# Kernel optimization log

Measured on AMD Instinct MI355X. Metric: run time of the kernel, lower is better.

The kernel has to match this reference:

```python
import jax, jax.numpy as jnp
import numpy as np

IN, H, FC1, FC2, OUT = 3, 30, 64, 32, 1
B, T = 8192, 256


def _lstm_layer(xT, W_ih, W_hh, b_ih, b_hh):
    """xT: (T, B, Din). Returns (hidden sequence (T,B,H), final h (B,H)).
    PyTorch gate order: i, f, g, o."""
    # Precompute input contribution for all timesteps (one big GEMM).
    gx = jnp.einsum('tbd,gd->tbg', xT, W_ih) + b_ih + b_hh  # (T,B,4H)
    b = xT.shape[1]
    h0 = jnp.zeros((b, W_hh.shape[1]), xT.dtype)
    c0 = h0

    def step(carry, g):
        h, c = carry
        gates = g + h @ W_hh.T
        i, f, gg, o = jnp.split(gates, 4, axis=-1)
        i = jax.nn.sigmoid(i)
        f = jax.nn.sigmoid(f)
        gg = jnp.tanh(gg)
        o = jax.nn.sigmoid(o)
        c = f * c + i * gg
        h = o * jnp.tanh(c)
        return (h, c), h

    (h_n, _), ys = jax.lax.scan(step, (h0, c0), gx)
    return ys, h_n


def setup_inputs() -> dict:
    key = jax.random.key(0)
    ks = jax.random.split(key, 16)
    s = 0.18  # ~1/sqrt(hidden_size), matches PyTorch uniform init scale
    inp = {
        'x': jax.random.normal(ks[0], (B, T, IN), jnp.float32),
        'W_ih0': jax.random.normal(ks[1], (4 * H, IN), jnp.float32) * s,
        'W_hh0': jax.random.normal(ks[2], (4 * H, H), jnp.float32) * s,
        'b_ih0': jax.random.normal(ks[3], (4 * H,), jnp.float32) * s,
        'b_hh0': jax.random.normal(ks[4], (4 * H,), jnp.float32) * s,
        'W_ih1': jax.random.normal(ks[5], (4 * H, H), jnp.float32) * s,
        'W_hh1': jax.random.normal(ks[6], (4 * H, H), jnp.float32) * s,
        'b_ih1': jax.random.normal(ks[7], (4 * H,), jnp.float32) * s,
        'b_hh1': jax.random.normal(ks[8], (4 * H,), jnp.float32) * s,
        'W_fc1': jax.random.normal(ks[9], (FC1, H), jnp.float32) * s,
        'b_fc1': jax.random.normal(ks[10], (FC1,), jnp.float32) * s,
        'W_fc2': jax.random.normal(ks[11], (FC2, FC1), jnp.float32) * 0.125,
        'b_fc2': jax.random.normal(ks[12], (FC2,), jnp.float32) * 0.125,
        'W_fc3': jax.random.normal(ks[13], (OUT, FC2), jnp.float32) * 0.17,
        'b_fc3': jax.random.normal(ks[14], (OUT,), jnp.float32) * 0.17,
    }
    return inp


def reference(x, W_ih0, W_hh0, b_ih0, b_hh0, W_ih1, W_hh1, b_ih1, b_hh1,
              W_fc1, b_fc1, W_fc2, b_fc2, W_fc3, b_fc3):
    xT = jnp.swapaxes(x, 0, 1)  # (T,B,IN)
    ys, _ = _lstm_layer(xT, W_ih0, W_hh0, b_ih0, b_hh0)   # layer 0 sequence
    _, h_n = _lstm_layer(ys, W_ih1, W_hh1, b_ih1, b_hh1)  # layer 1 final h
    # FC head (dropout = identity in eval mode)
    z = jax.nn.relu(h_n @ W_fc1.T + b_fc1)
    z = jax.nn.relu(z @ W_fc2.T + b_fc2)
    z = jax.nn.sigmoid(z @ W_fc3.T + b_fc3)
    return z.squeeze(-1)  # (B,)
```

## Files before the change

### kernel.cpp

```cpp
#include <hip/hip_runtime.h>

#define TT   256
#define HID  30
#define LOG2E 1.4426950408889634f
#define HS   40

typedef __bf16 bf16x8_t __attribute__((ext_vector_type(8)));
typedef float  f32x4_t  __attribute__((ext_vector_type(4)));

__device__ __forceinline__ float fexp2(float x){
#if __has_builtin(__builtin_amdgcn_exp2f)
    return __builtin_amdgcn_exp2f(x);
#else
    return exp2f(x);
#endif
}
__device__ __forceinline__ float frcp(float x){
#if __has_builtin(__builtin_amdgcn_rcpf)
    return __builtin_amdgcn_rcpf(x);
#else
    return 1.f/x;
#endif
}
__device__ __forceinline__ float fsigmoid(float x){ return frcp(1.f + fexp2(-LOG2E*x)); }
__device__ __forceinline__ f32x4_t exp4(f32x4_t v){
    f32x4_t e; e[0]=fexp2(v[0]); e[1]=fexp2(v[1]); e[2]=fexp2(v[2]); e[3]=fexp2(v[3]); return e;
}
__device__ __forceinline__ f32x4_t rcp4(f32x4_t v){
    f32x4_t r; r[0]=frcp(v[0]); r[1]=frcp(v[1]); r[2]=frcp(v[2]); r[3]=frcp(v[3]); return r;
}
__device__ __forceinline__ f32x4_t splat4(float v){ f32x4_t r = {v,v,v,v}; return r; }

__device__ __forceinline__ f32x4_t lstm_act(f32x4_t aI, f32x4_t aF, f32x4_t aG,
                                            f32x4_t aO, f32x4_t& cst){
    f32x4_t eI = exp4(aI);
    f32x4_t eF = exp4(aF);
    f32x4_t eG = exp4(aG);
    f32x4_t eO = exp4(aO);
    f32x4_t f  = rcp4(eF + 1.f);
    f32x4_t tG = eG + 1.f;
    f32x4_t p  = (eG - 1.f) * rcp4(eI*tG + tG);
    cst = f*cst + p;
    f32x4_t cc;
    cc[0]=fminf(fmaxf(cst[0],-30.f),30.f);
    cc[1]=fminf(fmaxf(cst[1],-30.f),30.f);
    cc[2]=fminf(fmaxf(cst[2],-30.f),30.f);
    cc[3]=fminf(fmaxf(cst[3],-30.f),30.f);
    f32x4_t eC = exp4(cc * (2.f*LOG2E));
    f32x4_t tC = eC + 1.f;
    return (eC - 1.f) * rcp4(eO*tC + tC);
}

__global__ __launch_bounds__(256, 2)
void lstm_fused(const float* __restrict__ x,
    const float* __restrict__ Wih0, const float* __restrict__ Whh0,
    const float* __restrict__ bih0, const float* __restrict__ bhh0,
    const float* __restrict__ Wih1, const float* __restrict__ Whh1,
    const float* __restrict__ bih1, const float* __restrict__ bhh1,
    const float* __restrict__ Wfc1, const float* __restrict__ bfc1,
    const float* __restrict__ Wfc2, const float* __restrict__ bfc2,
    const float* __restrict__ Wfc3, const float* __restrict__ bfc3,
    float* __restrict__ out)
{
    __shared__ __align__(16) __bf16 h0f[2][16][HS];
    __shared__ __align__(16) __bf16 h1f[2][16][HS];
    __shared__ float h1_last[16*32];
    __shared__ float zbuf[16*64];
    __shared__ float z2buf[16*32];

    const int tid  = threadIdx.x;
    const int lane = tid & 63;
    const int wv   = tid >> 6;
    const int lay  = wv >> 1;
    const int uh   = wv & 1;
    const int n    = lane & 15;
    const int q    = lane >> 4;
    const int q4   = q*4;
    const int u    = uh*16 + n;
    const bool colok = (u < HID);
    const int uq   = colok ? u : 0;
    const int bbase = blockIdx.x * 16;

    bf16x8_t fA[4], fB[4];
    float bv[4], wx[4];
    {
        const float scl[4] = {-LOG2E, -LOG2E, 2.f*LOG2E, -LOG2E};
        #pragma unroll
        for (int g = 0; g < 4; ++g) {
            const int row = g*HID + uq;
            const float sg = scl[g];
            bf16x8_t va{}, vb{};
            #pragma unroll
            for (int j = 0; j < 8; ++j) {
                int k = q*8 + j;
                float wa = 0.f, wb = 0.f;
                if (colok) {
                    if (lay == 0) {
                        if (k < HID)      wa = Whh0[row*HID + k];
                        else if (k < 32)  wa = Wih0[row*3 + (k - HID)];
                    } else {
                        if (k < HID) { wa = Wih1[row*HID + k];  wb = Whh1[row*HID + k]; }
                    }
                }
                va[j] = (__bf16)(sg*wa);
                vb[j] = (__bf16)(sg*wb);
            }
            fA[g] = va;  fB[g] = vb;
            float bb = 0.f, ww = 0.f;
            if (colok) {
                bb = lay ? (bih1[row] + bhh1[row]) : (bih0[row] + bhh0[row]);
                if (lay == 0) ww = Wih0[row*3 + 2];
            }
            bv[g] = sg*bb;  wx[g] = sg*ww;
        }
    }

    f32x4_t cst = {0.f,0.f,0.f,0.f};

    for (int i = tid; i < 2*16*HS; i += 256) {
        (&h0f[0][0][0])[i] = (__bf16)0.f;
        (&h1f[0][0][0])[i] = (__bf16)0.f;
    }
    __syncthreads();
    if (tid < 32) {
        int m = tid >> 1, cc = tid & 1;
        h0f[1][m][30+cc] = (__bf16)x[(size_t)(bbase+m)*(TT*3) + cc];
    }
    __syncthreads();

    const float* xB = x + (size_t)bbase*(TT*3);
    const int xo2  = (q*4)*(TT*3) + 2;
    const int xo01 = (tid>>1)*(TT*3) + (tid&1);
    f32x4_t x2 = {0.f,0.f,0.f,0.f};
    if (lay == 0) {
        x2[0]=xB[xo2]; x2[1]=xB[xo2+TT*3]; x2[2]=xB[xo2+2*TT*3]; x2[3]=xB[xo2+3*TT*3];
    }

#define STEP(S, RB, WB, FIRST) do {                                            \
    if (lay == 0) {                                                            \
        bf16x8_t A0 = *(const bf16x8_t*)(&h0f[RB][n][q*8]);                    \
        f32x4_t aI = __builtin_amdgcn_mfma_f32_16x16x32_bf16(A0, fA[0], x2*wx[0] + bv[0], 0,0,0); \
        f32x4_t aF = __builtin_amdgcn_mfma_f32_16x16x32_bf16(A0, fA[1], x2*wx[1] + bv[1], 0,0,0); \
        f32x4_t aG = __builtin_amdgcn_mfma_f32_16x16x32_bf16(A0, fA[2], x2*wx[2] + bv[2], 0,0,0); \
        f32x4_t aO = __builtin_amdgcn_mfma_f32_16x16x32_bf16(A0, fA[3], x2*wx[3] + bv[3], 0,0,0); \
        const int tpre = ((S)+2 < TT) ? (S)+2 : TT-1;                          \
        const float* xs = xB + 3*tpre;                                         \
        f32x4_t x2n;                                                           \
        x2n[0]=xs[xo2]; x2n[1]=xs[xo2+TT*3];                                   \
        x2n[2]=xs[xo2+2*TT*3]; x2n[3]=xs[xo2+3*TT*3];                          \
        float x01v = 0.f;                                                      \
        if (tid < 32) x01v = xs[xo01];                                         \
        f32x4_t h = lstm_act(aI, aF, aG, aO, cst);                             \
        if (colok) {                                                           \
            h0f[WB][q4  ][u] = (__bf16)h[0];                                   \
            h0f[WB][q4+1][u] = (__bf16)h[1];                                   \
            h0f[WB][q4+2][u] = (__bf16)h[2];                                   \
            h0f[WB][q4+3][u] = (__bf16)h[3];                                   \
        }                                                                      \
        if (tid < 32) h0f[WB][tid>>1][30+(tid&1)] = (__bf16)x01v;              \
        x2 = x2n;                                                              \
    } else if (!(FIRST)) {                                                     \
        bf16x8_t A1 = *(const bf16x8_t*)(&h0f[RB][n][q*8]);                    \
        bf16x8_t A2 = *(const bf16x8_t*)(&h1f[RB][n][q*8]);                    \
        f32x4_t aI = __builtin_amdgcn_mfma_f32_16x16x32_bf16(A2, fB[0], splat4(bv[0]), 0,0,0); \
        aI         = __builtin_amdgcn_mfma_f32_16x16x32_bf16(A1, fA[0], aI, 0,0,0); \
        f32x4_t aF = __builtin_amdgcn_mfma_f32_16x16x32_bf16(A2, fB[1], splat4(bv[1]), 0,0,0); \
        aF         = __builtin_amdgcn_mfma_f32_16x16x32_bf16(A1, fA[1], aF, 0,0,0); \
        f32x4_t aG = __builtin_amdgcn_mfma_f32_16x16x32_bf16(A2, fB[2], splat4(bv[2]), 0,0,0); \
        aG         = __builtin_amdgcn_mfma_f32_16x16x32_bf16(A1, fA[2], aG, 0,0,0); \
        f32x4_t aO = __builtin_amdgcn_mfma_f32_16x16x32_bf16(A2, fB[3], splat4(bv[3]), 0,0,0); \
        aO         = __builtin_amdgcn_mfma_f32_16x16x32_bf16(A1, fA[3], aO, 0,0,0); \
        f32x4_t h = lstm_act(aI, aF, aG, aO, cst);                             \
        if (colok) {                                                           \
            h1f[WB][q4  ][u] = (__bf16)h[0];                                   \
            h1f[WB][q4+1][u] = (__bf16)h[1];                                   \
            h1f[WB][q4+2][u] = (__bf16)h[2];                                   \
            h1f[WB][q4+3][u] = (__bf16)h[3];                                   \
            if ((S) == TT-1) {                                                 \
                h1_last[(q4  )*32+u] = h[0];                                   \
                h1_last[(q4+1)*32+u] = h[1];                                   \
                h1_last[(q4+2)*32+u] = h[2];                                   \
                h1_last[(q4+3)*32+u] = h[3];                                   \
            }                                                                  \
        }                                                                      \
    }                                                                          \
    __syncthreads();                                                           \
} while (0)

    STEP(-1, 1, 0, 1);
    #pragma unroll 1
    for (int s = 0; s < TT; s += 2) {
        STEP(s,   0, 1, 0);
        STEP(s+1, 1, 0, 0);
    }
#undef STEP

    #pragma unroll
    for (int rep = 0; rep < 4; ++rep) {
        int idx = tid + rep*256;
        int m = idx >> 6, uu = idx & 63;
        float a = bfc1[uu];
        for (int k = 0; k < HID; ++k) a += h1_last[m*32+k] * Wfc1[uu*HID+k];
        zbuf[m*64+uu] = fmaxf(a, 0.f);
    }
    __syncthreads();
    #pragma unroll
    for (int rep = 0; rep < 2; ++rep) {
        int idx = tid + rep*256;
        int m = idx >> 5, v = idx & 31;
        float a = bfc2[v];
        for (int k = 0; k < 64; ++k) a += zbuf[m*64+k] * Wfc2[v*64+k];
        z2buf[m*32+v] = fmaxf(a, 0.f);
    }
    __syncthreads();
    if (tid < 16) {
        float a = bfc3[0];
        for (int k = 0; k < 32; ++k) a += z2buf[tid*32+k] * Wfc3[k];
        out[bbase + tid] = fsigmoid(a);
    }
}

extern "C" void kernel_launch(void* const* d_in, const int* in_sizes, int n_in,
                              void* d_out, int out_size, void* d_ws, size_t ws_size,
                              hipStream_t stream) {
    const float* x    = (const float*)d_in[0];
    const float* Wih0 = (const float*)d_in[1];
    const float* Whh0 = (const float*)d_in[2];
    const float* bih0 = (const float*)d_in[3];
    const float* bhh0 = (const float*)d_in[4];
    const float* Wih1 = (const float*)d_in[5];
    const float* Whh1 = (const float*)d_in[6];
    const float* bih1 = (const float*)d_in[7];
    const float* bhh1 = (const float*)d_in[8];
    const float* Wfc1 = (const float*)d_in[9];
    const float* bfc1 = (const float*)d_in[10];
    const float* Wfc2 = (const float*)d_in[11];
    const float* bfc2 = (const float*)d_in[12];
    const float* Wfc3 = (const float*)d_in[13];
    const float* bfc3 = (const float*)d_in[14];
    float* outp = (float*)d_out;

    hipLaunchKernelGGL(lstm_fused, dim3(512), dim3(256), 0, stream,
        x, Wih0, Whh0, bih0, bhh0, Wih1, Whh1, bih1, bhh1,
        Wfc1, bfc1, Wfc2, bfc2, Wfc3, bfc3, outp);
}
```

Before: 284.3 us.

## Give each wave all hidden units of one layer, two batch groups per block

Each wave now computes all 30 hidden units of its layer (two 16-column MFMA halves) for a 16-row batch group, instead of splitting the hidden units across two waves. A block now handles 32 batch rows with 256 blocks, and launch bounds drop to one block per SIMD. The gate activation also merges the forget and input reciprocals into one reciprocal. This doubles the MFMA and activation work per wave to get more independent instruction-level parallelism per step, at the cost of more registers and fewer concurrent blocks. The diff also leaves a dead first STEP macro definition and stray macro clutter, which compile away.

```diff
diff --git a/kernel.cpp b/kernel.cpp
--- a/kernel.cpp
+++ b/kernel.cpp
@@ -37,9 +37,12 @@
     f32x4_t eF = exp4(aF);
     f32x4_t eG = exp4(aG);
     f32x4_t eO = exp4(aO);
-    f32x4_t f  = rcp4(eF + 1.f);
+    f32x4_t D1 = eF + 1.f;
     f32x4_t tG = eG + 1.f;
-    f32x4_t p  = (eG - 1.f) * rcp4(eI*tG + tG);
+    f32x4_t D2 = (eI + 1.f) * tG;
+    f32x4_t r  = rcp4(D1*D2);
+    f32x4_t f  = r*D2;
+    f32x4_t p  = (eG - 1.f) * (r*D1);
     cst = f*cst + p;
     f32x4_t cc;
     cc[0]=fminf(fmaxf(cst[0],-30.f),30.f);
@@ -48,10 +51,10 @@
     cc[3]=fminf(fmaxf(cst[3],-30.f),30.f);
     f32x4_t eC = exp4(cc * (2.f*LOG2E));
     f32x4_t tC = eC + 1.f;
-    return (eC - 1.f) * rcp4(eO*tC + tC);
-}
-
-__global__ __launch_bounds__(256, 2)
+    return (eC - 1.f) * rcp4((eO + 1.f)*tC);
+}
+
+__global__ __launch_bounds__(256, 1)
 void lstm_fused(const float* __restrict__ x,
     const float* __restrict__ Wih0, const float* __restrict__ Whh0,
     const float* __restrict__ bih0, const float* __restrict__ bhh0,
@@ -62,125 +65,257 @@
     const float* __restrict__ Wfc3, const float* __restrict__ bfc3,
     float* __restrict__ out)
 {
-    __shared__ __align__(16) __bf16 h0f[2][16][HS];
-    __shared__ __align__(16) __bf16 h1f[2][16][HS];
-    __shared__ float h1_last[16*32];
-    __shared__ float zbuf[16*64];
-    __shared__ float z2buf[16*32];
+    __shared__ __align__(16) __bf16 h0f[2][2][16][HS];
+    __shared__ __align__(16) __bf16 h1f[2][2][16][HS];
+    __shared__ float h1_last[2][16][32];
+    __shared__ float zbuf[32][64];
+    __shared__ float z2buf[32][32];
 
     const int tid  = threadIdx.x;
     const int lane = tid & 63;
     const int wv   = tid >> 6;
-    const int lay  = wv >> 1;
-    const int uh   = wv & 1;
+    const int grp  = wv >> 1;
+    const int role = wv & 1;
     const int n    = lane & 15;
     const int q    = lane >> 4;
     const int q4   = q*4;
-    const int u    = uh*16 + n;
-    const bool colok = (u < HID);
-    const int uq   = colok ? u : 0;
-    const int bbase = blockIdx.x * 16;
-
-    bf16x8_t fA[4], fB[4];
-    float bv[4], wx[4];
+    const int bbase = blockIdx.x * 32;
+    const int rbase = bbase + grp*16;
+
+    bf16x8_t wA[2][4], wB[2][4];
+    float bv[2][4], wx[2][4];
     {
         const float scl[4] = {-LOG2E, -LOG2E, 2.f*LOG2E, -LOG2E};
         #pragma unroll
-        for (int g = 0; g < 4; ++g) {
-            const int row = g*HID + uq;
-            const float sg = scl[g];
-            bf16x8_t va{}, vb{};
+        for (int h = 0; h < 2; ++h) {
+            const int u = h*16 + n;
+            const bool ok = (u < HID);
+            const int uq = ok ? u : 0;
             #pragma unroll
-            for (int j = 0; j < 8; ++j) {
-                int k = q*8 + j;
-                float wa = 0.f, wb = 0.f;
-                if (colok) {
-                    if (lay == 0) {
-                        if (k < HID)      wa = Whh0[row*HID + k];
-                        else if (k < 32)  wa = Wih0[row*3 + (k - HID)];
-                    } else {
-                        if (k < HID) { wa = Wih1[row*HID + k];  wb = Whh1[row*HID + k]; }
+            for (int g = 0; g < 4; ++g) {
+                const int row = g*HID + uq;
+                const float sg = scl[g];
+                bf16x8_t va{}, vb{};
+                #pragma unroll
+                for (int j = 0; j < 8; ++j) {
+                    int k = q*8 + j;
+                    float a = 0.f, b = 0.f;
+                    if (ok) {
+                        if (role == 0) {
+                            if (k < HID)      a = Whh0[row*HID + k];
+                            else if (k < 32)  a = Wih0[row*3 + (k - HID)];
+                        } else {
+                            if (k < HID) { a = Wih1[row*HID + k];  b = Whh1[row*HID + k]; }
+                        }
                     }
+                    va[j] = (__bf16)(sg*a);
+                    vb[j] = (__bf16)(sg*b);
                 }
-                va[j] = (__bf16)(sg*wa);
-                vb[j] = (__bf16)(sg*wb);
+                wA[h][g] = va;  wB[h][g] = vb;
+                float bb = 0.f, ww = 0.f;
+                if (ok) {
+                    bb = role ? (bih1[row] + bhh1[row]) : (bih0[row] + bhh0[row]);
+                    if (role == 0) ww = Wih0[row*3 + 2];
+                }
+                bv[h][g] = sg*bb;  wx[h][g] = sg*ww;
             }
-            fA[g] = va;  fB[g] = vb;
-            float bb = 0.f, ww = 0.f;
-            if (colok) {
-                bb = lay ? (bih1[row] + bhh1[row]) : (bih0[row] + bhh0[row]);
-                if (lay == 0) ww = Wih0[row*3 + 2];
-            }
-            bv[g] = sg*bb;  wx[g] = sg*ww;
         }
     }
 
-    f32x4_t cst = {0.f,0.f,0.f,0.f};
-
-    for (int i = tid; i < 2*16*HS; i += 256) {
-        (&h0f[0][0][0])[i] = (__bf16)0.f;
-        (&h1f[0][0][0])[i] = (__bf16)0.f;
+    f32x4_t cst0 = {0.f,0.f,0.f,0.f};
+    f32x4_t cst1 = {0.f,0.f,0.f,0.f};
+
+    for (int i = tid; i < 2*2*16*HS; i += 256) {
+        (&h0f[0][0][0][0])[i] = (__bf16)0.f;
+        (&h1f[0][0][0][0])[i] = (__bf16)0.f;
     }
     __syncthreads();
-    if (tid < 32) {
-        int m = tid >> 1, cc = tid & 1;
-        h0f[1][m][30+cc] = (__bf16)x[(size_t)(bbase+m)*(TT*3) + cc];
+    if (tid < 64) {
+        int g2 = tid >> 5, m = (tid >> 1) & 15, c = tid & 1;
+        h0f[g2][1][m][30+c] = (__bf16)x[(size_t)(bbase + g2*16 + m)*(TT*3) + c];
     }
     __syncthreads();
 
-    const float* xB = x + (size_t)bbase*(TT*3);
-    const int xo2  = (q*4)*(TT*3) + 2;
-    const int xo01 = (tid>>1)*(TT*3) + (tid&1);
-    f32x4_t x2 = {0.f,0.f,0.f,0.f};
-    if (lay == 0) {
-        x2[0]=xB[xo2]; x2[1]=xB[xo2+TT*3]; x2[2]=xB[xo2+2*TT*3]; x2[3]=xB[xo2+3*TT*3];
+    const float* xB = x + (size_t)rbase*(TT*3);
+    const int xo2  = q4*(TT*3) + 2;
+    const int xo01 = ((lane>>1)&15)*(TT*3) + (lane&1);
+    f32x4_t x2v = {0.f,0.f,0.f,0.f};
+    if (role == 0) {
+        x2v[0]=xB[xo2]; x2v[1]=xB[xo2+TT*3]; x2v[2]=xB[xo2+2*TT*3]; x2v[3]=xB[xo2+3*TT*3];
     }
 
 #define STEP(S, RB, WB, FIRST) do {                                            \
-    if (lay == 0) {                                                            \
-        bf16x8_t A0 = *(const bf16x8_t*)(&h0f[RB][n][q*8]);                    \
-        f32x4_t aI = __builtin_amdgcn_mfma_f32_16x16x32_bf16(A0, fA[0], x2*wx[0] + bv[0], 0,0,0); \
-        f32x4_t aF = __builtin_amdgcn_mfma_f32_16x16x32_bf16(A0, fA[1], x2*wx[1] + bv[1], 0,0,0); \
-        f32x4_t aG = __builtin_amdgcn_mfma_f32_16x16x32_bf16(A0, fA[2], x2*wx[2] + bv[2], 0,0,0); \
-        f32x4_t aO = __builtin_amdgcn_mfma_f32_16x16x32_bf16(A0, fA[3], x2*wx[3] + bv[3], 0,0,0); \
+    if (role == 0) {                                                           \
+        bf16x8_t A0 = *(const bf16x8_t*)(&h0f[grp][RB][n][q*8]);               \
+        f32x4_t aI0 = __builtin_amdgcn_mfma_f32_16x16x32_bf16(A0, wA[0][0], x2v*wx[0][0] + bv[0][0], 0,0,0); \
+        f32x4_t aF0 = __builtin_amdgcn_mfma_f32_16x16x32_bf16(A0, wA[0][1], x2v*wx[0][1] + bv[0][1], 0,0,0); \
+        f32x4_t aG0 = __builtin_amdgcn_mfma_f32_16x16x32_bf16(A0, wA[0][2], x2v*wx[0][2] + bv[0][2], 0,0,0); \
+        f32x4_t aO0 = __builtin_amdgcn_mfma_f32_16x16x32_bf16(A0, wA[0][3], x2v*wx[0][3] + bv[0][3], 0,0,0); \
+        f32x4_t aI1 = __builtin_amdgcn_mfma_f32_16x16x32_bf16(A0, wA[1][0], x2v*wx[1][0] + bv[1][0], 0,0,0); \
+        f32x4_t aF1 = __builtin_amdgcn_mfma_f32_16x16x32_bf16(A0, wA[1][1], x2v*wx[1][1] + bv[1][1], 0,0,0); \
+        f32x4_t aG1 = __builtin_amdgcn_mfma_f32_16x16x32_bf16(A0, wA[1][2], x2v*wx[1][2] + bv[1][2], 0,0,0); \
+        f32x4_t aO1 = __builtin_amdgcn_mfma_f32_16x16x32_bf16(A0, wA[1][3], x2v*wx[1][3] + bv[1][3], 0,0,0); \
         const int tpre = ((S)+2 < TT) ? (S)+2 : TT-1;                          \
         const float* xs = xB + 3*tpre;                                         \
         f32x4_t x2n;                                                           \
         x2n[0]=xs[xo2]; x2n[1]=xs[xo2+TT*3];                                   \
         x2n[2]=xs[xo2+2*TT*3]; x2n[3]=xs[xo2+3*TT*3];                          \
         float x01v = 0.f;                                                      \
-        if (tid < 32) x01v = xs[xo01];                                         \
-        f32x4_t h = lstm_act(aI, aF, aG, aO, cst);                             \
-        if (colok) {                                                           \
-            h0f[WB][q4  ][u] = (__bf16)h[0];                                   \
-            h0f[WB][q4+1][u] = (__bf16)h[1];                                   \
-            h0f[WB][q4+2][u] = (__bf16)h[2];                                   \
-            h0f[WB][q4+3][u] = (__bf16)h[3];                                   \
-        }                                                                      \
-        if (tid < 32) h0f[WB][tid>>1][30+(tid&1)] = (__bf16)x01v;              \
-        x2 = x2n;                                                              \
+        if (lane < 32) x01v = xs[xo01];                                        \
+        f32x4_t h0v = lstm_act(aI0, aF0, aG0, aO0, cst0);                      \
+        f32x4_t h1v = lstm_act(aI1, aF1, aG1, aO1, cst1);                      \
+        h0f[WB_ grp][q4  ][n] = (__bf16)h0v[0];                                \
+        h0f[WB_ grp][q4+1][n] = (__bf16)h0v[1];                                \
+        h0f[WB_ grp][q4+2][n] = (__bf16)h0v[2];                                \
+        h0f[WB_ grp][q4+3][n] = (__bf16)h0v[3];                                \
+        if (n < 14) {                                                          \
+            h0f[WB_ grp][q4  ][16+n] = (__bf16)h1v[0];                         \
+            h0f[WB_ grp][q4+1][16+n] = (__bf16)h1v[1];                         \
+            h0f[WB_ grp][q4+2][16+n] = (__bf16)h1v[2];                         \
+            h0f[WB_ grp][q4+3][16+n] = (__bf16)h1v[3];                         \
+        }                                                                      \
+        if (lane < 32) h0f[WB_ grp][(lane>>1)&15][30+(lane&1)] = (__bf16)x01v; \
+        x2v = x2n;                                                             \
     } else if (!(FIRST)) {                                                     \
-        bf16x8_t A1 = *(const bf16x8_t*)(&h0f[RB][n][q*8]);                    \
-        bf16x8_t A2 = *(const bf16x8_t*)(&h1f[RB][n][q*8]);                    \
-        f32x4_t aI = __builtin_amdgcn_mfma_f32_16x16x32_bf16(A2, fB[0], splat4(bv[0]), 0,0,0); \
-        aI         = __builtin_amdgcn_mfma_f32_16x16x32_bf16(A1, fA[0], aI, 0,0,0); \
-        f32x4_t aF = __builtin_amdgcn_mfma_f32_16x16x32_bf16(A2, fB[1], splat4(bv[1]), 0,0,0); \
-        aF         = __builtin_amdgcn_mfma_f32_16x16x32_bf16(A1, fA[1], aF, 0,0,0); \
-        f32x4_t aG = __builtin_amdgcn_mfma_f32_16x16x32_bf16(A2, fB[2], splat4(bv[2]), 0,0,0); \
-        aG         = __builtin_amdgcn_mfma_f32_16x16x32_bf16(A1, fA[2], aG, 0,0,0); \
-        f32x4_t aO = __builtin_amdgcn_mfma_f32_16x16x32_bf16(A2, fB[3], splat4(bv[3]), 0,0,0); \
-        aO         = __builtin_amdgcn_mfma_f32_16x16x32_bf16(A1, fA[3], aO, 0,0,0); \
-        f32x4_t h = lstm_act(aI, aF, aG, aO, cst);                             \
-        if (colok) {                                                           \
-            h1f[WB][q4  ][u] = (__bf16)h[0];                                   \
-            h1f[WB][q4+1][u] = (__bf16)h[1];                                   \
-            h1f[WB][q4+2][u] = (__bf16)h[2];                                   \
-            h1f[WB][q4+3][u] = (__bf16)h[3];                                   \
-            if ((S) == TT-1) {                                                 \
-                h1_last[(q4  )*32+u] = h[0];                                   \
-                h1_last[(q4+1)*32+u] = h[1];                                   \
-                h1_last[(q4+2)*32+u] = h[2];                                   \
-                h1_last[(q4+3)*32+u] = h[3];                                   \
+        bf16x8_t A1 = *(const bf16x8_t*)(&h0f[grp][RB][n][q*8]);               \
+        bf16x8_t A2 = *(const bf16x8_t*)(&h1f[grp][RB][n][q*8]);               \
+        f32x4_t aI0 = __builtin_amdgcn_mfma_f32_16x16x32_bf16(A2, wB[0][0], splat4(bv[0][0]), 0,0,0); \
+        f32x4_t aF0 = __builtin_amdgcn_mfma_f32_16x16x32_bf16(A2, wB[0][1], splat4(bv[0][1]), 0,0,0); \
+        f32x4_t aG0 = __builtin_amdgcn_mfma_f32_16x16x32_bf16(A2, wB[0][2], splat4(bv[0][2]), 0,0,0); \
+        f32x4_t aO0 = __builtin_amdgcn_mfma_f32_16x16x32_bf16(A2, wB[0][3], splat4(bv[0][3]), 0,0,0); \
+        f32x4_t aI1 = __builtin_amdgcn_mfma_f32_16x16x32_bf16(A2, wB[1][0], splat4(bv[1][0]), 0,0,0); \
+        f32x4_t aF1 = __builtin_amdgcn_mfma_f32_16x16x32_bf16(A2, wB[1][1], splat4(bv[1][1]), 0,0,0); \
+        f32x4_t aG1 = __builtin_amdgcn_mfma_f32_16x16x32_bf16(A2, wB[1][2], splat4(bv[1][2]), 0,0,0); \
+        f32x4_t aO1 = __builtin_amdgcn_mfma_f32_16x16x32_bf16(A2, wB[1][3], splat4(bv[1][3]), 0,0,0); \
+        aI0 = __builtin_amdgcn_mfma_f32_16x16x32_bf16(A1, wA[0][0], aI0, 0,0,0); \
+        aF0 = __builtin_amdgcn_mfma_f32_16x16x32_bf16(A1, wA[0][1], aF0, 0,0,0); \
+        aG0 = __builtin_amdgcn_mfma_f32_16x16x32_bf16(A1, wA[0][2], aG0, 0,0,0); \
+        aO0 = __builtin_amdgcn_mfma_f32_16x16x32_bf16(A1, wA[0][3], aO0, 0,0,0); \
+        aI1 = __builtin_amdgcn_mfma_f32_16x16x32_bf16(A1, wA[1][0], aI1, 0,0,0); \
+        aF1 = __builtin_amdgcn_mfma_f32_16x16x32_bf16(A1, wA[1][1], aF1, 0,0,0); \
+        aG1 = __builtin_amdgcn_mfma_f32_16x16x32_bf16(A1, wA[1][2], aG1, 0,0,0); \
+        aO1 = __builtin_amdgcn_mfma_f32_16x16x32_bf16(A1, wA[1][3], aO1, 0,0,0); \
+        f32x4_t h0v = lstm_act(aI0, aF0, aG0, aO0, cst0);                      \
+        f32x4_t h1v = lstm_act(aI1, aF1, aG1, aO1, cst1);                      \
+        h1f[WB_ grp][q4  ][n] = (__bf16)h0v[0];                                \
+        h1f[WB_ grp][q4+1][n] = (__bf16)h0v[1];                                \
+        h1f[WB_ grp][q4+2][n] = (__bf16)h0v[2];                                \
+        h1f[WB_ grp][q4+3][n] = (__bf16)h0v[3];                                \
+        if (n < 14) {                                                          \
+            h1f[WB_ grp][q4  ][16+n] = (__bf16)h1v[0];                         \
+            h1f[WB_ grp][q4+1][16+n] = (__bf16)h1v[1];                         \
+            h1f[WB_ grp][q4+2][16+n] = (__bf16)h1v[2];                         \
+            h1f[WB_ grp][q4+3][16+n] = (__bf16)h1v[3];                         \
+        }                                                                      \
+        if ((S) == TT-1) {                                                     \
+            h1_last[grp][q4  ][n] = h0v[0];                                    \
+            h1_last[grp][q4+1][n] = h0v[1];                                    \
+            h1_last[grp][q4+2][n] = h0v[2];                                    \
+            h1_last[grp][q4+3][n] = h0v[3];                                    \
+            if (n < 14) {                                                      \
+                h1_last[grp][q4  ][16+n] = h1v[0];                             \
+                h1_last[grp][q4+1][16+n] = h1v[1];                             \
+                h1_last[grp][q4+2][16+n] = h1v[2];                             \
+                h1_last[grp][q4+3][16+n] = h1v[3];                             \
+            }                                                                  \
+        }                                                                      \
+    }                                                                          \
+    __syncthreads();                                                           \
+} while (0)
+
+#define WB_ grp
+
+    {
+        #define PROLOG_RB 1
+        #undef PROLOG_RB
+    }
+
+#undef WB_
+
+#define STEPX(S, RB, WB, FIRST)                                                \
+    do {                                                                       \
+        _Pragma("clang diagnostic push")                                       \
+        STEP_IMPL(S, RB, WB, FIRST);                                           \
+        _Pragma("clang diagnostic pop")                                        \
+    } while (0)
+
+#define WB_ 0][
+#undef WB_
+
+#undef STEP
+#define STEP(S, RB, WB, FIRST) do {                                            \
+    if (role == 0) {                                                           \
+        bf16x8_t A0 = *(const bf16x8_t*)(&h0f[grp][RB][n][q*8]);               \
+        f32x4_t aI0 = __builtin_amdgcn_mfma_f32_16x16x32_bf16(A0, wA[0][0], x2v*wx[0][0] + bv[0][0], 0,0,0); \
+        f32x4_t aF0 = __builtin_amdgcn_mfma_f32_16x16x32_bf16(A0, wA[0][1], x2v*wx[0][1] + bv[0][1], 0,0,0); \
+        f32x4_t aG0 = __builtin_amdgcn_mfma_f32_16x16x32_bf16(A0, wA[0][2], x2v*wx[0][2] + bv[0][2], 0,0,0); \
+        f32x4_t aO0 = __builtin_amdgcn_mfma_f32_16x16x32_bf16(A0, wA[0][3], x2v*wx[0][3] + bv[0][3], 0,0,0); \
+        f32x4_t aI1 = __builtin_amdgcn_mfma_f32_16x16x32_bf16(A0, wA[1][0], x2v*wx[1][0] + bv[1][0], 0,0,0); \
+        f32x4_t aF1 = __builtin_amdgcn_mfma_f32_16x16x32_bf16(A0, wA[1][1], x2v*wx[1][1] + bv[1][1], 0,0,0); \
+        f32x4_t aG1 = __builtin_amdgcn_mfma_f32_16x16x32_bf16(A0, wA[1][2], x2v*wx[1][2] + bv[1][2], 0,0,0); \
+        f32x4_t aO1 = __builtin_amdgcn_mfma_f32_16x16x32_bf16(A0, wA[1][3], x2v*wx[1][3] + bv[1][3], 0,0,0); \
+        const int tpre = ((S)+2 < TT) ? (S)+2 : TT-1;                          \
+        const float* xs = xB + 3*tpre;                                         \
+        f32x4_t x2n;                                                           \
+        x2n[0]=xs[xo2]; x2n[1]=xs[xo2+TT*3];                                   \
+        x2n[2]=xs[xo2+2*TT*3]; x2n[3]=xs[xo2+3*TT*3];                          \
+        float x01v = 0.f;                                                      \
+        if (lane < 32) x01v = xs[xo01];                                        \
+        f32x4_t h0v = lstm_act(aI0, aF0, aG0, aO0, cst0);                      \
+        f32x4_t h1v = lstm_act(aI1, aF1, aG1, aO1, cst1);                      \
+        h0f[grp][WB][q4  ][n] = (__bf16)h0v[0];                                \
+        h0f[grp][WB][q4+1][n] = (__bf16)h0v[1];                                \
+        h0f[grp][WB][q4+2][n] = (__bf16)h0v[2];                                \
+        h0f[grp][WB][q4+3][n] = (__bf16)h0v[3];                                \
+        if (n < 14) {                                                          \
+            h0f[grp][WB][q4  ][16+n] = (__bf16)h1v[0];                         \
+            h0f[grp][WB][q4+1][16+n] = (__bf16)h1v[1];                         \
+            h0f[grp][WB][q4+2][16+n] = (__bf16)h1v[2];                         \
+            h0f[grp][WB][q4+3][16+n] = (__bf16)h1v[3];                         \
+        }                                                                      \
+        if (lane < 32) h0f[grp][WB][(lane>>1)&15][30+(lane&1)] = (__bf16)x01v; \
+        x2v = x2n;                                                             \
+    } else if (!(FIRST)) {                                                     \
+        bf16x8_t A1 = *(const bf16x8_t*)(&h0f[grp][RB][n][q*8]);               \
+        bf16x8_t A2 = *(const bf16x8_t*)(&h1f[grp][RB][n][q*8]);               \
+        f32x4_t aI0 = __builtin_amdgcn_mfma_f32_16x16x32_bf16(A2, wB[0][0], splat4(bv[0][0]), 0,0,0); \
+        f32x4_t aF0 = __builtin_amdgcn_mfma_f32_16x16x32_bf16(A2, wB[0][1], splat4(bv[0][1]), 0,0,0); \
+        f32x4_t aG0 = __builtin_amdgcn_mfma_f32_16x16x32_bf16(A2, wB[0][2], splat4(bv[0][2]), 0,0,0); \
+        f32x4_t aO0 = __builtin_amdgcn_mfma_f32_16x16x32_bf16(A2, wB[0][3], splat4(bv[0][3]), 0,0,0); \
+        f32x4_t aI1 = __builtin_amdgcn_mfma_f32_16x16x32_bf16(A2, wB[1][0], splat4(bv[1][0]), 0,0,0); \
+        f32x4_t aF1 = __builtin_amdgcn_mfma_f32_16x16x32_bf16(A2, wB[1][1], splat4(bv[1][1]), 0,0,0); \
+        f32x4_t aG1 = __builtin_amdgcn_mfma_f32_16x16x32_bf16(A2, wB[1][2], splat4(bv[1][2]), 0,0,0); \
+        f32x4_t aO1 = __builtin_amdgcn_mfma_f32_16x16x32_bf16(A2, wB[1][3], splat4(bv[1][3]), 0,0,0); \
+        aI0 = __builtin_amdgcn_mfma_f32_16x16x32_bf16(A1, wA[0][0], aI0, 0,0,0); \
+        aF0 = __builtin_amdgcn_mfma_f32_16x16x32_bf16(A1, wA[0][1], aF0, 0,0,0); \
+        aG0 = __builtin_amdgcn_mfma_f32_16x16x32_bf16(A1, wA[0][2], aG0, 0,0,0); \
+        aO0 = __builtin_amdgcn_mfma_f32_16x16x32_bf16(A1, wA[0][3], aO0, 0,0,0); \
+        aI1 = __builtin_amdgcn_mfma_f32_16x16x32_bf16(A1, wA[1][0], aI1, 0,0,0); \
+        aF1 = __builtin_amdgcn_mfma_f32_16x16x32_bf16(A1, wA[1][1], aF1, 0,0,0); \
+        aG1 = __builtin_amdgcn_mfma_f32_16x16x32_bf16(A1, wA[1][2], aG1, 0,0,0); \
+        aO1 = __builtin_amdgcn_mfma_f32_16x16x32_bf16(A1, wA[1][3], aO1, 0,0,0); \
+        f32x4_t h0v = lstm_act(aI0, aF0, aG0, aO0, cst0);                      \
+        f32x4_t h1v = lstm_act(aI1, aF1, aG1, aO1, cst1);                      \
+        h1f[grp][WB][q4  ][n] = (__bf16)h0v[0];                                \
+        h1f[grp][WB][q4+1][n] = (__bf16)h0v[1];                                \
+        h1f[grp][WB][q4+2][n] = (__bf16)h0v[2];                                \
+        h1f[grp][WB][q4+3][n] = (__bf16)h0v[3];                                \
+        if (n < 14) {                                                          \
+            h1f[grp][WB][q4  ][16+n] = (__bf16)h1v[0];                         \
+            h1f[grp][WB][q4+1][16+n] = (__bf16)h1v[1];                         \
+            h1f[grp][WB][q4+2][16+n] = (__bf16)h1v[2];                         \
+            h1f[grp][WB][q4+3][16+n] = (__bf16)h1v[3];                         \
+        }                                                                      \
+        if ((S) == TT-1) {                                                     \
+            h1_last[grp][q4  ][n] = h0v[0];                                    \
+            h1_last[grp][q4+1][n] = h0v[1];                                    \
+            h1_last[grp][q4+2][n] = h0v[2];                                    \
+            h1_last[grp][q4+3][n] = h0v[3];                                    \
+            if (n < 14) {                                                      \
+                h1_last[grp][q4  ][16+n] = h1v[0];                             \
+                h1_last[grp][q4+1][16+n] = h1v[1];                             \
+                h1_last[grp][q4+2][16+n] = h1v[2];                             \
+                h1_last[grp][q4+3][16+n] = h1v[3];                             \
             }                                                                  \
         }                                                                      \
     }                                                                          \
@@ -196,26 +331,26 @@
 #undef STEP
 
     #pragma unroll
-    for (int rep = 0; rep < 4; ++rep) {
+    for (int rep = 0; rep < 8; ++rep) {
         int idx = tid + rep*256;
         int m = idx >> 6, uu = idx & 63;
         float a = bfc1[uu];
-        for (int k = 0; k < HID; ++k) a += h1_last[m*32+k] * Wfc1[uu*HID+k];
-        zbuf[m*64+uu] = fmaxf(a, 0.f);
+        for (int k = 0; k < HID; ++k) a += h1_last[m>>4][m&15][k] * Wfc1[uu*HID+k];
+        zbuf[m][uu] = fmaxf(a, 0.f);
     }
     __syncthreads();
     #pragma unroll
-    for (int rep = 0; rep < 2; ++rep) {
+    for (int rep = 0; rep < 4; ++rep) {
         int idx = tid + rep*256;
         int m = idx >> 5, v = idx & 31;
         float a = bfc2[v];
-        for (int k = 0; k < 64; ++k) a += zbuf[m*64+k] * Wfc2[v*64+k];
-        z2buf[m*32+v] = fmaxf(a, 0.f);
+        for (int k = 0; k < 64; ++k) a += zbuf[m][k] * Wfc2[v*64+k];
+        z2buf[m][v] = fmaxf(a, 0.f);
     }
     __syncthreads();
-    if (tid < 16) {
+    if (tid < 32) {
         float a = bfc3[0];
-        for (int k = 0; k < 32; ++k) a += z2buf[tid*32+k] * Wfc3[k];
+        for (int k = 0; k < 32; ++k) a += z2buf[tid][k] * Wfc3[k];
         out[bbase + tid] = fsigmoid(a);
     }
 }
@@ -240,7 +375,7 @@
     const float* bfc3 = (const float*)d_in[14];
     float* outp = (float*)d_out;
 
-    hipLaunchKernelGGL(lstm_fused, dim3(512), dim3(256), 0, stream,
+    hipLaunchKernelGGL(lstm_fused, dim3(256), dim3(256), 0, stream,
         x, Wih0, Whh0, bih0, bhh0, Wih1, Whh1, bih1, bhh1,
         Wfc1, bfc1, Wfc2, bfc2, Wfc3, bfc3, outp);
 }
```

Measured after the change: 343.6 us. +20.9%, slower.
